# Performance work log

Measured on AMD Instinct MI355X. Metric: run time of the kernel, lower is better.

The kernel has to match this reference:

```python
import jax, jax.numpy as jnp
import numpy as np

N = 20000   # num_nodes
D = 128     # node_dim
H = 128     # hidden_dim (also per-head channels, PyG out_channels is per-head)
EV = 64     # event_dim
NH = 4      # heads
E = 250000  # num edges
NT = 8      # num_event_types
K = 4       # active event types


def setup_inputs() -> dict:
    key = jax.random.key(0)
    ks = jax.random.split(key, 24)
    def w(i, shape, s=0.05):
        return jax.random.normal(ks[i], shape, dtype=jnp.float32) * s
    z = lambda shape: jnp.zeros(shape, jnp.float32)
    o = lambda shape: jnp.ones(shape, jnp.float32)
    return {
        "node_ids": jnp.arange(N, dtype=jnp.int32),
        "event_type_ids": jax.random.randint(ks[0], (K,), 0, NT, dtype=jnp.int32),
        "src": jax.random.randint(ks[1], (E,), 0, N, dtype=jnp.int32),
        "dst": jax.random.randint(ks[2], (E,), 0, N, dtype=jnp.int32),
        "event_features": jax.random.normal(ks[3], (EV,), dtype=jnp.float32),
        "event_intensity": jax.random.uniform(ks[4], (K,), dtype=jnp.float32),
        "node_emb_table": w(5, (N, D), 1.0),
        "event_type_table": w(6, (NT, H), 0.5),
        "ev_w1": w(7, (EV, H)), "ev_b1": z((H,)), "ev_g1": o((H,)), "ev_bt1": z((H,)),
        "ev_w2": w(8, (H, H)), "ev_b2": z((H,)), "ev_g2": o((H,)), "ev_bt2": z((H,)),
        "wq": w(9, (D + H, NH * H)), "bq": z((NH * H,)),
        "wk": w(10, (D + H, NH * H)), "bk": z((NH * H,)),
        "wv": w(11, (D + H, NH * H)), "bv": z((NH * H,)),
        "wskip": w(12, (D + H, H)), "bskip": z((H,)),
        "g0_w": w(13, (H, NH * H)), "g0_as": w(14, (NH, H), 0.1), "g0_ad": w(15, (NH, H), 0.1), "g0_b": z((H,)),
        "g1_w": w(16, (H, NH * H)), "g1_as": w(17, (NH, H), 0.1), "g1_ad": w(18, (NH, H), 0.1), "g1_b": z((H,)),
        "wih": w(19, (H, 4 * H)), "whh": w(20, (H, 4 * H)), "bih": z((4 * H,)), "bhh": z((4 * H,)),
    }


def layer_norm(x, g, b, eps=1e-5):
    mu = jnp.mean(x, axis=-1, keepdims=True)
    var = jnp.mean(jnp.square(x - mu), axis=-1, keepdims=True)
    return (x - mu) * jax.lax.rsqrt(var + eps) * g + b


def segment_softmax(logits, seg, n):
    # logits: [E, NH]; softmax over edges sharing the same destination seg id
    m = jax.ops.segment_max(logits, seg, num_segments=n)
    m = jnp.where(jnp.isfinite(m), m, 0.0)  # guard empty segments
    e = jnp.exp(logits - m[seg])
    s = jax.ops.segment_sum(e, seg, num_segments=n)
    return e / (s[seg] + 1e-16)


def _forward(node_ids, event_type_ids, src, dst,
             event_features, event_intensity, node_emb_table, event_type_table,
             ev_w1, ev_b1, ev_g1, ev_bt1, ev_w2, ev_b2, ev_g2, ev_bt2,
             wq, bq, wk, bk, wv, bv, wskip, bskip,
             g0_w, g0_as, g0_ad, g0_b, g1_w, g1_as, g1_ad, g1_b,
             wih, whh, bih, bhh):
    node_emb = node_emb_table[node_ids]                                      # [N, D]
    # event encoder MLP (dropout off / eval mode)
    e = jax.nn.relu(layer_norm(event_features @ ev_w1 + ev_b1, ev_g1, ev_bt1))
    e = jax.nn.relu(layer_norm(e @ ev_w2 + ev_b2, ev_g2, ev_bt2))            # [H]
    # intensity-weighted mean of active event-type embeddings
    e = e + jnp.mean(event_type_table[event_type_ids] * event_intensity[:, None], axis=0)
    x = jnp.concatenate([node_emb, jnp.broadcast_to(e, (N, H))], axis=1)     # [N, D+H]

    # --- TransformerConv (heads=NH, concat=False -> head mean, root_weight skip) ---
    q = (x @ wq + bq).reshape(N, NH, H)
    k = (x @ wk + bk).reshape(N, NH, H)
    v = (x @ wv + bv).reshape(N, NH, H)
    alpha = jnp.sum(q[dst] * k[src], axis=-1) / jnp.sqrt(jnp.float32(H))     # [E, NH]
    alpha = segment_softmax(alpha, dst, N)
    agg = jax.ops.segment_sum(v[src] * alpha[..., None], dst, num_segments=N)  # [N, NH, H]
    x = agg.mean(axis=1) + x @ wskip + bskip                                 # [N, H]

    sl = jnp.arange(N, dtype=src.dtype)
    src2 = jnp.concatenate([src, sl])
    dst2 = jnp.concatenate([dst, sl])
    for w_, asrc, adst, b_ in ((g0_w, g0_as, g0_ad, g0_b), (g1_w, g1_as, g1_ad, g1_b)):
        xh = (x @ w_).reshape(N, NH, H)
        a_s = jnp.sum(xh * asrc, axis=-1)                                    # [N, NH]
        a_d = jnp.sum(xh * adst, axis=-1)
        ee = jax.nn.leaky_relu(a_s[src2] + a_d[dst2], 0.2)                   # [E+N, NH]
        a = segment_softmax(ee, dst2, N)
        out = jax.ops.segment_sum(xh[src2] * a[..., None], dst2, num_segments=N)
        x = jax.nn.relu(out.mean(axis=1) + b_)                               # [N, H]

    # --- batched LSTMCell, zero initial (h, c); torch gate order i, f, g, o ---
    h0 = jnp.zeros((N, H), x.dtype)
    c0 = jnp.zeros((N, H), x.dtype)
    gates = x @ wih + bih + h0 @ whh + bhh                                   # [N, 4H]
    gi, gf, gg, go = jnp.split(gates, 4, axis=-1)
    c = jax.nn.sigmoid(gf) * c0 + jax.nn.sigmoid(gi) * jnp.tanh(gg)
    h = jax.nn.sigmoid(go) * jnp.tanh(c)
    return h, c


def reference(node_ids, event_type_ids, src, dst,
              event_features, event_intensity, node_emb_table, event_type_table,
              ev_w1, ev_b1, ev_g1, ev_bt1, ev_w2, ev_b2, ev_g2, ev_bt2,
              wq, bq, wk, bk, wv, bv, wskip, bskip,
              g0_w, g0_as, g0_ad, g0_b, g1_w, g1_as, g1_ad, g1_b,
              wih, whh, bih, bhh):
    return _forward(node_ids, event_type_ids, src, dst,
                    event_features, event_intensity, node_emb_table, event_type_table,
                    ev_w1, ev_b1, ev_g1, ev_bt1, ev_w2, ev_b2, ev_g2, ev_bt2,
                    wq, bq, wk, bk, wv, bv, wskip, bskip,
                    g0_w, g0_as, g0_ad, g0_b, g1_w, g1_as, g1_ad, g1_b,
                    wih, whh, bih, bhh)
```

## Files before the change

### kernel.cpp

```cpp
#include <hip/hip_runtime.h>
#include <math.h>

#define D_DIM 128
#define H_DIM 128
#define SQRT_H_INV 0.08838834764831845f
#define BCOL_QKV 0
#define BCOL_G0 1664
#define BCOL_G1 2176
#define BCOL_W  2688
#define BCOL_TOT 3072

typedef unsigned short u16;
typedef unsigned int u32;
typedef unsigned short ushort8v __attribute__((ext_vector_type(8)));
typedef unsigned int u32x4 __attribute__((ext_vector_type(4)));
typedef __bf16 bf16x8 __attribute__((ext_vector_type(8)));
typedef float f32x4 __attribute__((ext_vector_type(4)));
typedef float f32x2 __attribute__((ext_vector_type(2)));


__device__ __forceinline__ float grp16_sum(float v) {
  v += __shfl_xor(v, 1);
  v += __shfl_xor(v, 2);
  v += __shfl_xor(v, 4);
  v += __shfl_xor(v, 8);
  return v;
}

__device__ __forceinline__ void split_bf16(float x, u16& h, u16& l) {
  __bf16 hb = (__bf16)x;
  float rm = x - (float)hb;
  __bf16 lb = (__bf16)rm;
  h = __builtin_bit_cast(u16, hb);
  l = __builtin_bit_cast(u16, lb);
}

__device__ __forceinline__ f32x2 cvt2(u32 v) {
  f32x2 r;
  r[0] = __builtin_bit_cast(float, v << 16);
  r[1] = __builtin_bit_cast(float, v & 0xffff0000u);
  return r;
}

__device__ __forceinline__ float qk_dot(const u32x4 q, const u32x4 k) {
  float p = 0.f;
  asm("v_dot2_f32_bf16 %0, %1, %2, %0" : "+v"(p) : "v"(q[0]), "v"(k[0]));
  asm("v_dot2_f32_bf16 %0, %1, %2, %0" : "+v"(p) : "v"(q[1]), "v"(k[1]));
  asm("v_dot2_f32_bf16 %0, %1, %2, %0" : "+v"(p) : "v"(q[2]), "v"(k[2]));
  asm("v_dot2_f32_bf16 %0, %1, %2, %0" : "+v"(p) : "v"(q[3]), "v"(k[3]));
  return p;
}

__global__ __launch_bounds__(128) void k_event(
    const float* __restrict__ ef, int EV,
    const float* __restrict__ w1, const float* __restrict__ b1,
    const float* __restrict__ g1, const float* __restrict__ bt1,
    const float* __restrict__ w2, const float* __restrict__ b2,
    const float* __restrict__ g2, const float* __restrict__ bt2,
    const float* __restrict__ ett, const int* __restrict__ etid,
    const float* __restrict__ inten, int K,
    float* __restrict__ e_out)
{
  __shared__ float sh[H_DIM];
  __shared__ float red[H_DIM];
  const int t = threadIdx.x;

  float acc = b1[t];
  for (int i = 0; i < EV; ++i) acc += ef[i] * w1[i * H_DIM + t];

  red[t] = acc; __syncthreads();
  for (int s = 64; s > 0; s >>= 1) { if (t < s) red[t] += red[t + s]; __syncthreads(); }
  float mu = red[0] / H_DIM; __syncthreads();
  float d = acc - mu;
  red[t] = d * d; __syncthreads();
  for (int s = 64; s > 0; s >>= 1) { if (t < s) red[t] += red[t + s]; __syncthreads(); }
  float var = red[0] / H_DIM; __syncthreads();
  float y = d * rsqrtf(var + 1e-5f) * g1[t] + bt1[t];
  y = fmaxf(y, 0.f);
  sh[t] = y; __syncthreads();

  float acc2 = b2[t];
  for (int i = 0; i < H_DIM; ++i) acc2 += sh[i] * w2[i * H_DIM + t];

  red[t] = acc2; __syncthreads();
  for (int s = 64; s > 0; s >>= 1) { if (t < s) red[t] += red[t + s]; __syncthreads(); }
  mu = red[0] / H_DIM; __syncthreads();
  d = acc2 - mu;
  red[t] = d * d; __syncthreads();
  for (int s = 64; s > 0; s >>= 1) { if (t < s) red[t] += red[t + s]; __syncthreads(); }
  var = red[0] / H_DIM; __syncthreads();
  float y2 = d * rsqrtf(var + 1e-5f) * g2[t] + bt2[t];
  y2 = fmaxf(y2, 0.f);

  float m = 0.f;
  for (int k = 0; k < K; ++k) m += ett[etid[k] * H_DIM + t] * inten[k];
  e_out[t] = y2 + m / (float)K;
}

__global__ __launch_bounds__(256) void k_cvec_all(
    const float* __restrict__ e,
    const float* __restrict__ wq, const float* __restrict__ bq,
    const float* __restrict__ wk, const float* __restrict__ bk,
    const float* __restrict__ wv, const float* __restrict__ bv,
    const float* __restrict__ wskip, const float* __restrict__ bskip,
    const float* __restrict__ bih, const float* __restrict__ bhh,
    float* __restrict__ cvec1, float* __restrict__ cvec2)
{
  __shared__ float es[H_DIM];
  const int t = threadIdx.x;
  if (t < H_DIM) es[t] = e[t];
  __syncthreads();
  int j = blockIdx.x * 256 + t;
  if (j < 1664) {
    const float* W; const float* b; int col; int stride;
    if (j < 512)       { W = wq;    b = bq;    col = j;        stride = 512; }
    else if (j < 1024) { W = wk;    b = bk;    col = j - 512;  stride = 512; }
    else if (j < 1536) { W = wv;    b = bv;    col = j - 1024; stride = 512; }
    else               { W = wskip; b = bskip; col = j - 1536; stride = 128; }
    float a = b[col];
    for (int i = 0; i < H_DIM; ++i) a += es[i] * W[(D_DIM + i) * stride + col];
    cvec1[j] = a;
  } else if (j < 1664 + 384) {
    int j2 = j - 1664;
    int src = (j2 < 128) ? j2 : j2 + 128;
    cvec2[j2] = bih[src] + bhh[src];
  }
}

__global__ __launch_bounds__(256) void k_split_all(
    const float* __restrict__ wq, const float* __restrict__ wk,
    const float* __restrict__ wv, const float* __restrict__ wskip,
    const float* __restrict__ g0w, const float* __restrict__ g1w,
    const float* __restrict__ wih,
    u16* __restrict__ hi, u16* __restrict__ lo)
{
  int idx = blockIdx.x * 256 + threadIdx.x;
  if (idx >= BCOL_TOT * 16) return;
  int n = idx >> 4, g = idx & 15;
  const float* W; int col, stride;
  if (n < 512)        { W = wq;    col = n;        stride = 512; }
  else if (n < 1024)  { W = wk;    col = n - 512;  stride = 512; }
  else if (n < 1536)  { W = wv;    col = n - 1024; stride = 512; }
  else if (n < 1664)  { W = wskip; col = n - 1536; stride = 128; }
  else if (n < 2176)  { W = g0w;   col = n - 1664; stride = 512; }
  else if (n < 2688)  { W = g1w;   col = n - 2176; stride = 512; }
  else { int c = n - 2688; W = wih; col = (c < 128) ? c : c + 128; stride = 512; }
  size_t dst = (size_t)(n >> 4) * 2048 + g * 128 + (n & 15) * 8;
#pragma unroll
  for (int j = 0; j < 8; ++j) {
    u16 h, l;
    split_bf16(W[(size_t)(g * 8 + j) * stride + col], h, l);
    hi[dst + j] = h; lo[dst + j] = l;
  }
}

__global__ __launch_bounds__(256) void k_split_a(
    const float* __restrict__ A, const int* __restrict__ ids,
    u16* __restrict__ hi, u16* __restrict__ lo, int M, int Mpad)
{
  int idx = blockIdx.x * 256 + threadIdx.x;
  if (idx >= Mpad * 16) return;
  int row = idx >> 4, g = idx & 15;
  size_t dst = (size_t)(row >> 4) * 2048 + g * 128 + (row & 15) * 8;
  if (row < M) {
    int ar = ids ? ids[row] : row;
    const float* srcp = A + (size_t)ar * 128 + g * 8;
#pragma unroll
    for (int j = 0; j < 8; ++j) {
      u16 h, l;
      split_bf16(srcp[j], h, l);
      hi[dst + j] = h; lo[dst + j] = l;
    }
  } else {
#pragma unroll
    for (int j = 0; j < 8; ++j) { hi[dst + j] = 0; lo[dst + j] = 0; }
  }
}

__global__ __launch_bounds__(256, 3) void mfma_gemm(
    const u16* __restrict__ Ahi, const u16* __restrict__ Alo,
    const u16* __restrict__ Bhi, const u16* __restrict__ Blo,
    const float* __restrict__ cvec,
    u16* __restrict__ bf_out, int bf_cols,
    float* __restrict__ f32_out, int f32_lo, int ld_f32,
    const float* __restrict__ asw, const float* __restrict__ adw,
    float* __restrict__ a_s, float* __restrict__ a_d,
    int M)
{
  __shared__ float red[256];

  const int t = threadIdx.x;
  const int bm = blockIdx.y * 128;
  const int bn = blockIdx.x * 128;
  const int lane = t & 63;
  const int wid = t >> 6;
  const int wr = wid >> 1, wc = wid & 1;
  const int lg = lane >> 4;
  const int lr = lane & 15;

  const int arb = (bm >> 4) + wr * 4;
  const int brb = (bn >> 4) + wc * 4;

  f32x4 acc[4][4];
  const f32x4 zero = {0.f, 0.f, 0.f, 0.f};
#pragma unroll
  for (int i = 0; i < 4; ++i)
#pragma unroll
    for (int j = 0; j < 4; ++j) acc[i][j] = zero;

#pragma unroll
  for (int ks = 0; ks < 4; ++ks) {
    const int g = ks * 4 + lg;
    bf16x8 ah[4], al[4], bh[4], bl[4];
#pragma unroll
    for (int i = 0; i < 4; ++i) {
      size_t oa = (size_t)(arb + i) * 2048 + g * 128 + lr * 8;
      ah[i] = *(const bf16x8*)&Ahi[oa];
      al[i] = *(const bf16x8*)&Alo[oa];
      size_t ob = (size_t)(brb + i) * 2048 + g * 128 + lr * 8;
      bh[i] = *(const bf16x8*)&Bhi[ob];
      bl[i] = *(const bf16x8*)&Blo[ob];
    }
#pragma unroll
    for (int i = 0; i < 4; ++i)
#pragma unroll
      for (int j = 0; j < 4; ++j) {
        acc[i][j] = __builtin_amdgcn_mfma_f32_16x16x32_bf16(ah[i], bh[j], acc[i][j], 0, 0, 0);
        acc[i][j] = __builtin_amdgcn_mfma_f32_16x16x32_bf16(ah[i], bl[j], acc[i][j], 0, 0, 0);
        acc[i][j] = __builtin_amdgcn_mfma_f32_16x16x32_bf16(al[i], bh[j], acc[i][j], 0, 0, 0);
      }
  }

  const int rq = (lane >> 4) << 2;
  const int cq = lane & 15;
  const int head = bn >> 7;

  float ws_[4], wd_[4];
  if (asw) {
#pragma unroll
    for (int j = 0; j < 4; ++j) {
      int cc = (wc * 64 + j * 16 + cq) & 127;
      ws_[j] = asw[head * 128 + cc];
      wd_[j] = adw[head * 128 + cc];
    }
    if (t < 256) red[t] = 0.f;
    __syncthreads();
  }

#pragma unroll
  for (int i = 0; i < 4; ++i) {
#pragma unroll
    for (int r = 0; r < 4; ++r) {
      int rowl = wr * 64 + i * 16 + rq + r;
      int row = bm + rowl;
      bool rok = row < M;
      float ps = 0.f, pd = 0.f;
#pragma unroll
      for (int j = 0; j < 4; ++j) {
        int col = bn + wc * 64 + j * 16 + cq;
        float a = acc[i][j][r];
        if (rok) {
          float val = a + (cvec ? cvec[col] : 0.f);
          if (bf_out && col < bf_cols)
            bf_out[(size_t)row * bf_cols + col] =
                __builtin_bit_cast(u16, (__bf16)val);
          if (f32_out && col >= f32_lo)
            f32_out[(size_t)row * ld_f32 + (col - f32_lo)] = val;
        }
        if (asw) { ps += a * ws_[j]; pd += a * wd_[j]; }
      }
      if (asw && rok) {
        atomicAdd(&red[rowl], ps);
        atomicAdd(&red[128 + rowl], pd);
      }
    }
  }
  if (asw) {
    __syncthreads();
    if (t < 128) {
      int row = bm + t;
      if (row < M) {
        a_s[row * 4 + head] = red[t];
        a_d[row * 4 + head] = red[128 + t];
      }
    }
  }
}

__global__ __launch_bounds__(256) void k_zero(int* __restrict__ p, int n) {
  int i = blockIdx.x * 256 + threadIdx.x;
  if (i < n) p[i] = 0;
}
__global__ __launch_bounds__(256) void k_count(
    const int* __restrict__ dst, int* __restrict__ counts, int E) {
  int e = blockIdx.x * 256 + threadIdx.x;
  if (e < E) atomicAdd(&counts[dst[e]], 1);
}
__global__ __launch_bounds__(1024) void k_scan(
    const int* __restrict__ counts, int* __restrict__ offs,
    int* __restrict__ cursor, int N)
{
  __shared__ int wsum[16];
  const int t = threadIdx.x;
  const int lane = t & 63;
  const int wid = t >> 6;
  int running = 0;
  for (int base = 0; base < N; base += 1024) {
    int v = (base + t < N) ? counts[base + t] : 0;
    int incl = v;
#pragma unroll
    for (int s = 1; s < 64; s <<= 1) {
      int u = __shfl_up(incl, s);
      if (lane >= s) incl += u;
    }
    if (lane == 63) wsum[wid] = incl;
    __syncthreads();
    if (wid == 0) {
      int w = (lane < 16) ? wsum[lane] : 0;
#pragma unroll
      for (int s = 1; s < 16; s <<= 1) {
        int u = __shfl_up(w, s);
        if (lane >= s) w += u;
      }
      if (lane < 16) wsum[lane] = w;
    }
    __syncthreads();
    int wpre = (wid > 0) ? wsum[wid - 1] : 0;
    int tot = wsum[15];
    int inclg = incl + wpre;
    if (base + t < N) {
      offs[base + t + 1] = running + inclg;
      cursor[base + t] = running + inclg - v;
    }
    running += tot;
    __syncthreads();
  }
  if (t == 0) offs[0] = 0;
}
__global__ __launch_bounds__(256) void k_fill(
    const int* __restrict__ src, const int* __restrict__ dst,
    int* __restrict__ cursor, int* __restrict__ csr_src, int E) {
  int e = blockIdx.x * 256 + threadIdx.x;
  if (e < E) {
    int slot = atomicAdd(&cursor[dst[e]], 1);
    csr_src[slot] = src[e];
  }
}

__global__ __launch_bounds__(256) void k_tconv(
    const u16* __restrict__ QKVp, const float* __restrict__ skipbuf,
    const int* __restrict__ offs, const int* __restrict__ csr_src,
    u16* __restrict__ Xhi, u16* __restrict__ Xlo, int N)
{
  const int wid = threadIdx.x >> 6;
  const int lane = threadIdx.x & 63;
  const int node = blockIdx.x * 4 + wid;
  if (node >= N) {
    if (lane < 16) {
      size_t dst = (size_t)(node >> 4) * 2048 + lane * 128 + (node & 15) * 8;
#pragma unroll
      for (int j = 0; j < 8; ++j) { Xhi[dst + j] = 0; Xlo[dst + j] = 0; }
    }
    return;
  }
  const u32x4 q = *(const u32x4*)(QKVp + (size_t)node * 1536 + lane * 8);

  const int beg = offs[node], end = offs[node + 1];
  float mx = -1e30f;
  float ssum = 0.f;
  f32x2 acc2[4];
#pragma unroll
  for (int jj = 0; jj < 4; ++jj) acc2[jj] = (f32x2){0.f, 0.f};

  int e = beg;
  for (; e + 4 <= end; e += 4) {
    int s0 = csr_src[e];
    int s1 = csr_src[e + 1];
    int s2 = csr_src[e + 2];
    int s3 = csr_src[e + 3];
    const u16* r0 = QKVp + (size_t)s0 * 1536 + 512 + lane * 8;
    const u16* r1 = QKVp + (size_t)s1 * 1536 + 512 + lane * 8;
    const u16* r2 = QKVp + (size_t)s2 * 1536 + 512 + lane * 8;
    const u16* r3 = QKVp + (size_t)s3 * 1536 + 512 + lane * 8;
    u32x4 k0 = *(const u32x4*)(r0);
    u32x4 k1 = *(const u32x4*)(r1);
    u32x4 k2 = *(const u32x4*)(r2);
    u32x4 k3 = *(const u32x4*)(r3);
    u32x4 v0 = *(const u32x4*)(r0 + 512);
    u32x4 v1 = *(const u32x4*)(r1 + 512);
    u32x4 v2 = *(const u32x4*)(r2 + 512);
    u32x4 v3 = *(const u32x4*)(r3 + 512);
    float p0 = qk_dot(q, k0);
    float p1 = qk_dot(q, k1);
    float p2 = qk_dot(q, k2);
    float p3 = qk_dot(q, k3);
    p0 = grp16_sum(p0) * SQRT_H_INV;
    p1 = grp16_sum(p1) * SQRT_H_INV;
    p2 = grp16_sum(p2) * SQRT_H_INV;
    p3 = grp16_sum(p3) * SQRT_H_INV;
    float pmax = fmaxf(fmaxf(p0, p1), fmaxf(p2, p3));
    if (!__all(pmax <= mx)) {
      float nm = fmaxf(mx, pmax);
      float sc = expf(mx - nm);
      f32x2 sc2 = {sc, sc};
      ssum *= sc;
#pragma unroll
      for (int jj = 0; jj < 4; ++jj) acc2[jj] *= sc2;
      mx = nm;
    }
    float w0 = expf(p0 - mx);
    float w1 = expf(p1 - mx);
    float w2 = expf(p2 - mx);
    float w3 = expf(p3 - mx);
    ssum += (w0 + w1) + (w2 + w3);
    f32x2 w02 = {w0, w0}, w12 = {w1, w1}, w22 = {w2, w2}, w32 = {w3, w3};
#pragma unroll
    for (int jj = 0; jj < 4; ++jj)
      acc2[jj] = acc2[jj] + (w02 * cvt2(v0[jj]) + w12 * cvt2(v1[jj]))
                          + (w22 * cvt2(v2[jj]) + w32 * cvt2(v3[jj]));
  }
  for (; e < end; ++e) {
    int s0 = csr_src[e];
    const u16* r0 = QKVp + (size_t)s0 * 1536 + 512 + lane * 8;
    u32x4 k0 = *(const u32x4*)(r0);
    u32x4 v0 = *(const u32x4*)(r0 + 512);
    float p0 = qk_dot(q, k0);
    p0 = grp16_sum(p0) * SQRT_H_INV;
    if (!__all(p0 <= mx)) {
      float nm = fmaxf(mx, p0);
      float sc = expf(mx - nm);
      f32x2 sc2 = {sc, sc};
      ssum *= sc;
#pragma unroll
      for (int jj = 0; jj < 4; ++jj) acc2[jj] *= sc2;
      mx = nm;
    }
    float w0 = expf(p0 - mx);
    ssum += w0;
    f32x2 w02 = {w0, w0};
#pragma unroll
    for (int jj = 0; jj < 4; ++jj)
      acc2[jj] = acc2[jj] + w02 * cvt2(v0[jj]);
  }

  float inv = 1.f / (ssum + 1e-16f);
  float acc[8];
#pragma unroll
  for (int jj = 0; jj < 4; ++jj) {
    acc[jj * 2]     = acc2[jj][0] * inv;
    acc[jj * 2 + 1] = acc2[jj][1] * inv;
  }
#pragma unroll
  for (int j = 0; j < 8; ++j) {
    acc[j] += __shfl_xor(acc[j], 16);
    acc[j] += __shfl_xor(acc[j], 32);
  }
  if (lane < 16) {
    const float* sk = skipbuf + (size_t)node * 128 + lane * 8;
    size_t dst = (size_t)(node >> 4) * 2048 + lane * 128 + (node & 15) * 8;
#pragma unroll
    for (int j = 0; j < 8; ++j) {
      float x = 0.25f * acc[j] + sk[j];
      u16 h, l;
      split_bf16(x, h, l);
      Xhi[dst + j] = h; Xlo[dst + j] = l;
    }
  }
}

__global__ __launch_bounds__(256) void k_gat_agg(
    const u16* __restrict__ xhb,
    const float* __restrict__ a_s, const float* __restrict__ a_d,
    const int* __restrict__ offs, const int* __restrict__ csr_src,
    const float* __restrict__ bias,
    u16* __restrict__ Xhi, u16* __restrict__ Xlo, int N)
{
  const int wid = threadIdx.x >> 6;
  const int lane = threadIdx.x & 63;
  const int node = blockIdx.x * 4 + wid;
  if (node >= N) {
    if (lane < 16) {
      size_t dst = (size_t)(node >> 4) * 2048 + lane * 128 + (node & 15) * 8;
#pragma unroll
      for (int j = 0; j < 8; ++j) { Xhi[dst + j] = 0; Xlo[dst + j] = 0; }
    }
    return;
  }
  const int head = lane >> 4;
  const float adn = a_d[node * 4 + head];
  const float asn = a_s[node * 4 + head];
  float lself = asn + adn;
  lself = lself >= 0.f ? lself : 0.2f * lself;

  float mx = lself;
  float ssum = 1.f;
  f32x2 acc2[4];
  {
    u32x4 xs = *(const u32x4*)(xhb + (size_t)node * 512 + lane * 8);
#pragma unroll
    for (int jj = 0; jj < 4; ++jj) acc2[jj] = cvt2(xs[jj]);
  }

  const int beg = offs[node], end = offs[node + 1];
  int e = beg;
  for (; e + 4 <= end; e += 4) {
    int s0 = csr_src[e];
    int s1 = csr_src[e + 1];
    int s2 = csr_src[e + 2];
    int s3 = csr_src[e + 3];
    float l0 = a_s[s0 * 4 + head];
    float l1 = a_s[s1 * 4 + head];
    float l2 = a_s[s2 * 4 + head];
    float l3 = a_s[s3 * 4 + head];
    const u16* r0 = xhb + (size_t)s0 * 512 + lane * 8;
    const u16* r1 = xhb + (size_t)s1 * 512 + lane * 8;
    const u16* r2 = xhb + (size_t)s2 * 512 + lane * 8;
    const u16* r3 = xhb + (size_t)s3 * 512 + lane * 8;
    u32x4 xa = *(const u32x4*)(r0);
    u32x4 xb = *(const u32x4*)(r1);
    u32x4 xc = *(const u32x4*)(r2);
    u32x4 xd = *(const u32x4*)(r3);
    l0 += adn; l1 += adn; l2 += adn; l3 += adn;
    l0 = l0 >= 0.f ? l0 : 0.2f * l0;
    l1 = l1 >= 0.f ? l1 : 0.2f * l1;
    l2 = l2 >= 0.f ? l2 : 0.2f * l2;
    l3 = l3 >= 0.f ? l3 : 0.2f * l3;
    float lmax = fmaxf(fmaxf(l0, l1), fmaxf(l2, l3));
    if (!__all(lmax <= mx)) {
      float nm = fmaxf(mx, lmax);
      float sc = expf(mx - nm);
      f32x2 sc2 = {sc, sc};
      ssum *= sc;
#pragma unroll
      for (int jj = 0; jj < 4; ++jj) acc2[jj] *= sc2;
      mx = nm;
    }
    float w0 = expf(l0 - mx);
    float w1 = expf(l1 - mx);
    float w2 = expf(l2 - mx);
    float w3 = expf(l3 - mx);
    ssum += (w0 + w1) + (w2 + w3);
    f32x2 w02 = {w0, w0}, w12 = {w1, w1}, w22 = {w2, w2}, w32 = {w3, w3};
#pragma unroll
    for (int jj = 0; jj < 4; ++jj)
      acc2[jj] = acc2[jj] + (w02 * cvt2(xa[jj]) + w12 * cvt2(xb[jj]))
                          + (w22 * cvt2(xc[jj]) + w32 * cvt2(xd[jj]));
  }
  for (; e < end; ++e) {
    int s0 = csr_src[e];
    float l0 = a_s[s0 * 4 + head] + adn;
    l0 = l0 >= 0.f ? l0 : 0.2f * l0;
    const u16* r0 = xhb + (size_t)s0 * 512 + lane * 8;
    u32x4 xa = *(const u32x4*)(r0);
    if (!__all(l0 <= mx)) {
      float nm = fmaxf(mx, l0);
      float sc = expf(mx - nm);
      f32x2 sc2 = {sc, sc};
      ssum *= sc;
#pragma unroll
      for (int jj = 0; jj < 4; ++jj) acc2[jj] *= sc2;
      mx = nm;
    }
    float w0 = expf(l0 - mx);
    ssum += w0;
    f32x2 w02 = {w0, w0};
#pragma unroll
    for (int jj = 0; jj < 4; ++jj)
      acc2[jj] = acc2[jj] + w02 * cvt2(xa[jj]);
  }

  float inv = 1.f / (ssum + 1e-16f);
  float acc[8];
#pragma unroll
  for (int jj = 0; jj < 4; ++jj) {
    acc[jj * 2]     = acc2[jj][0] * inv;
    acc[jj * 2 + 1] = acc2[jj][1] * inv;
  }
#pragma unroll
  for (int j = 0; j < 8; ++j) {
    acc[j] += __shfl_xor(acc[j], 16);
    acc[j] += __shfl_xor(acc[j], 32);
  }
  if (lane < 16) {
    const float* b = bias + lane * 8;
    size_t dst = (size_t)(node >> 4) * 2048 + lane * 128 + (node & 15) * 8;
#pragma unroll
    for (int j = 0; j < 8; ++j) {
      float x = fmaxf(0.25f * acc[j] + b[j], 0.f);
      u16 h, l;
      split_bf16(x, h, l);
      Xhi[dst + j] = h; Xlo[dst + j] = l;
    }
  }
}

__global__ __launch_bounds__(256) void k_lstm(
    const float* __restrict__ gates, float* __restrict__ out, int N)
{
  int idx = blockIdx.x * 256 + threadIdx.x;
  if (idx >= N * 128) return;
  int n = idx >> 7, c = idx & 127;
  const float* g = gates + (size_t)n * 384;
  float gi = g[c], gg = g[128 + c], go = g[256 + c];
  float cv = (1.f / (1.f + expf(-gi))) * tanhf(gg);
  float hv = (1.f / (1.f + expf(-go))) * tanhf(cv);
  out[idx] = hv;
  out[(size_t)N * 128 + idx] = cv;
}

extern "C" void kernel_launch(void* const* d_in, const int* in_sizes, int n_in,
                              void* d_out, int out_size, void* d_ws, size_t ws_size,
                              hipStream_t stream) {
  const int*   node_ids = (const int*)d_in[0];
  const int*   etid     = (const int*)d_in[1];
  const int*   src      = (const int*)d_in[2];
  const int*   dst      = (const int*)d_in[3];
  const float* ef       = (const float*)d_in[4];
  const float* inten    = (const float*)d_in[5];
  const float* nemb     = (const float*)d_in[6];
  const float* ett      = (const float*)d_in[7];
  const float* ev_w1 = (const float*)d_in[8],  *ev_b1 = (const float*)d_in[9];
  const float* ev_g1 = (const float*)d_in[10], *ev_bt1 = (const float*)d_in[11];
  const float* ev_w2 = (const float*)d_in[12], *ev_b2 = (const float*)d_in[13];
  const float* ev_g2 = (const float*)d_in[14], *ev_bt2 = (const float*)d_in[15];
  const float* wq = (const float*)d_in[16], *bq = (const float*)d_in[17];
  const float* wk = (const float*)d_in[18], *bk = (const float*)d_in[19];
  const float* wv = (const float*)d_in[20], *bv = (const float*)d_in[21];
  const float* wskip = (const float*)d_in[22], *bskip = (const float*)d_in[23];
  const float* g0_w = (const float*)d_in[24], *g0_as = (const float*)d_in[25];
  const float* g0_ad = (const float*)d_in[26], *g0_b = (const float*)d_in[27];
  const float* g1_w = (const float*)d_in[28], *g1_as = (const float*)d_in[29];
  const float* g1_ad = (const float*)d_in[30], *g1_b = (const float*)d_in[31];
  const float* wih = (const float*)d_in[32];
  const float* bih = (const float*)d_in[34], *bhh = (const float*)d_in[35];

  const int N = in_sizes[0];
  const int K = in_sizes[1];
  const int E = in_sizes[2];
  const int EV = in_sizes[4];

  const int gridMy = (N + 127) / 128;
  const int Npad = gridMy * 128;

  float* ws = (float*)d_ws;
  size_t o = 0;
  float* e_vec = ws + o; o += 128;
  float* cvec1 = ws + o; o += 1664;
  float* cvec2 = ws + o; o += 384;
  u16* Ballhi = (u16*)(ws + o); o += (size_t)BCOL_TOT * 64;
  u16* Balllo = (u16*)(ws + o); o += (size_t)BCOL_TOT * 64;
  u16* Ahi  = (u16*)(ws + o); o += (size_t)Npad * 64;
  u16* Alo  = (u16*)(ws + o); o += (size_t)Npad * 64;
  u16* XShi = (u16*)(ws + o); o += (size_t)Npad * 64;
  u16* XSlo = (u16*)(ws + o); o += (size_t)Npad * 64;
  u16* QKVp = (u16*)(ws + o); o += (size_t)Npad * 768;
  float* skipbuf = ws + o; o += (size_t)Npad * 128;
  u16* xhb  = (u16*)(ws + o); o += (size_t)Npad * 256;
  float* gates = ws + o; o += (size_t)Npad * 192;
  float* a_s   = ws + o; o += (size_t)N * 4;
  float* a_d   = ws + o; o += (size_t)N * 4;
  int* counts  = (int*)(ws + o); o += N;
  int* offs    = (int*)(ws + o); o += (size_t)N + 1;
  int* cursor  = (int*)(ws + o); o += N;
  int* csr_src = (int*)(ws + o); o += E;

  float* out = (float*)d_out;
  const int nodeBlocksPad = Npad / 4;

  k_event<<<1, 128, 0, stream>>>(ef, EV, ev_w1, ev_b1, ev_g1, ev_bt1,
                                 ev_w2, ev_b2, ev_g2, ev_bt2,
                                 ett, etid, inten, K, e_vec);
  k_cvec_all<<<8, 256, 0, stream>>>(e_vec, wq, bq, wk, bk, wv, bv,
                                    wskip, bskip, bih, bhh, cvec1, cvec2);
  k_split_all<<<(BCOL_TOT * 16) / 256, 256, 0, stream>>>(
      wq, wk, wv, wskip, g0_w, g1_w, wih, Ballhi, Balllo);
  k_split_a<<<(Npad * 16 + 255) / 256, 256, 0, stream>>>(nemb, node_ids, Ahi, Alo, N, Npad);

  k_zero<<<(N + 255) / 256, 256, 0, stream>>>(counts, N);
  k_count<<<(E + 255) / 256, 256, 0, stream>>>(dst, counts, E);
  k_scan<<<1, 1024, 0, stream>>>(counts, offs, cursor, N);
  k_fill<<<(E + 255) / 256, 256, 0, stream>>>(src, dst, cursor, csr_src, E);

  mfma_gemm<<<dim3(13, gridMy), 256, 0, stream>>>(
      Ahi, Alo, Ballhi + (size_t)BCOL_QKV * 128, Balllo + (size_t)BCOL_QKV * 128,
      cvec1, QKVp, 1536, skipbuf, 1536, 128,
      nullptr, nullptr, nullptr, nullptr, N);

  k_tconv<<<nodeBlocksPad, 256, 0, stream>>>(QKVp, skipbuf, offs, csr_src,
                                             XShi, XSlo, N);

  mfma_gemm<<<dim3(4, gridMy), 256, 0, stream>>>(
      XShi, XSlo, Ballhi + (size_t)BCOL_G0 * 128, Balllo + (size_t)BCOL_G0 * 128,
      nullptr, xhb, 512, nullptr, 0, 0,
      g0_as, g0_ad, a_s, a_d, N);
  k_gat_agg<<<nodeBlocksPad, 256, 0, stream>>>(xhb, a_s, a_d, offs, csr_src,
                                               g0_b, XShi, XSlo, N);

  mfma_gemm<<<dim3(4, gridMy), 256, 0, stream>>>(
      XShi, XSlo, Ballhi + (size_t)BCOL_G1 * 128, Balllo + (size_t)BCOL_G1 * 128,
      nullptr, xhb, 512, nullptr, 0, 0,
      g1_as, g1_ad, a_s, a_d, N);
  k_gat_agg<<<nodeBlocksPad, 256, 0, stream>>>(xhb, a_s, a_d, offs, csr_src,
                                               g1_b, XShi, XSlo, N);

  mfma_gemm<<<dim3(3, gridMy), 256, 0, stream>>>(
      XShi, XSlo, Ballhi + (size_t)BCOL_W * 128, Balllo + (size_t)BCOL_W * 128,
      cvec2, nullptr, 0, gates, 0, 384,
      nullptr, nullptr, nullptr, nullptr, N);
  k_lstm<<<((N * 128) + 255) / 256, 256, 0, stream>>>(gates, out, N);
}
```

Baseline: 461.2 us.

## Use persistent work-stealing waves for attention aggregation kernels

```diff
diff --git a/kernel.cpp b/kernel.cpp
--- a/kernel.cpp
+++ b/kernel.cpp
@@ -49,6 +49,12 @@
   asm("v_dot2_f32_bf16 %0, %1, %2, %0" : "+v"(p) : "v"(q[2]), "v"(k[2]));
   asm("v_dot2_f32_bf16 %0, %1, %2, %0" : "+v"(p) : "v"(q[3]), "v"(k[3]));
   return p;
+}
+
+__device__ __forceinline__ int steal(int* ctr, int lane) {
+  int n = 0;
+  if (lane == 0) n = atomicAdd(ctr, 1);
+  return __shfl(n, 0);
 }
 
 __global__ __launch_bounds__(128) void k_event(
@@ -350,120 +356,113 @@
 __global__ __launch_bounds__(256) void k_tconv(
     const u16* __restrict__ QKVp, const float* __restrict__ skipbuf,
     const int* __restrict__ offs, const int* __restrict__ csr_src,
-    u16* __restrict__ Xhi, u16* __restrict__ Xlo, int N)
-{
-  const int wid = threadIdx.x >> 6;
+    u16* __restrict__ Xhi, u16* __restrict__ Xlo, int N, int Npad,
+    int* __restrict__ wctr)
+{
   const int lane = threadIdx.x & 63;
-  const int node = blockIdx.x * 4 + wid;
-  if (node >= N) {
-    if (lane < 16) {
-      size_t dst = (size_t)(node >> 4) * 2048 + lane * 128 + (node & 15) * 8;
-#pragma unroll
-      for (int j = 0; j < 8; ++j) { Xhi[dst + j] = 0; Xlo[dst + j] = 0; }
-    }
-    return;
-  }
-  const u32x4 q = *(const u32x4*)(QKVp + (size_t)node * 1536 + lane * 8);
-
-  const int beg = offs[node], end = offs[node + 1];
-  float mx = -1e30f;
-  float ssum = 0.f;
-  f32x2 acc2[4];
-#pragma unroll
-  for (int jj = 0; jj < 4; ++jj) acc2[jj] = (f32x2){0.f, 0.f};
-
-  int e = beg;
-  for (; e + 4 <= end; e += 4) {
-    int s0 = csr_src[e];
-    int s1 = csr_src[e + 1];
-    int s2 = csr_src[e + 2];
-    int s3 = csr_src[e + 3];
-    const u16* r0 = QKVp + (size_t)s0 * 1536 + 512 + lane * 8;
-    const u16* r1 = QKVp + (size_t)s1 * 1536 + 512 + lane * 8;
-    const u16* r2 = QKVp + (size_t)s2 * 1536 + 512 + lane * 8;
-    const u16* r3 = QKVp + (size_t)s3 * 1536 + 512 + lane * 8;
-    u32x4 k0 = *(const u32x4*)(r0);
-    u32x4 k1 = *(const u32x4*)(r1);
-    u32x4 k2 = *(const u32x4*)(r2);
-    u32x4 k3 = *(const u32x4*)(r3);
-    u32x4 v0 = *(const u32x4*)(r0 + 512);
-    u32x4 v1 = *(const u32x4*)(r1 + 512);
-    u32x4 v2 = *(const u32x4*)(r2 + 512);
-    u32x4 v3 = *(const u32x4*)(r3 + 512);
-    float p0 = qk_dot(q, k0);
-    float p1 = qk_dot(q, k1);
-    float p2 = qk_dot(q, k2);
-    float p3 = qk_dot(q, k3);
-    p0 = grp16_sum(p0) * SQRT_H_INV;
-    p1 = grp16_sum(p1) * SQRT_H_INV;
-    p2 = grp16_sum(p2) * SQRT_H_INV;
-    p3 = grp16_sum(p3) * SQRT_H_INV;
-    float pmax = fmaxf(fmaxf(p0, p1), fmaxf(p2, p3));
-    if (!__all(pmax <= mx)) {
-      float nm = fmaxf(mx, pmax);
+
+  for (;;) {
+    const int node = steal(wctr, lane);
+    if (node >= Npad) return;
+    if (node >= N) {
+      if (lane < 16) {
+        size_t dst = (size_t)(node >> 4) * 2048 + lane * 128 + (node & 15) * 8;
+#pragma unroll
+        for (int j = 0; j < 8; ++j) { Xhi[dst + j] = 0; Xlo[dst + j] = 0; }
+      }
+      continue;
+    }
+    const u32x4 q = *(const u32x4*)(QKVp + (size_t)node * 1536 + lane * 8);
+
+    const int beg = offs[node], end = offs[node + 1];
+    float mx = -1e30f;
+    float ssum = 0.f;
+    f32x2 acc2[4];
+#pragma unroll
+    for (int jj = 0; jj < 4; ++jj) acc2[jj] = (f32x2){0.f, 0.f};
+
+    int e = beg;
+    for (; e + 4 <= end; e += 4) {
+      int s0 = csr_src[e];
+      int s1 = csr_src[e + 1];
+      int s2 = csr_src[e + 2];
+      int s3 = csr_src[e + 3];
+      const u16* r0 = QKVp + (size_t)s0 * 1536 + 512 + lane * 8;
+      const u16* r1 = QKVp + (size_t)s1 * 1536 + 512 + lane * 8;
+      const u16* r2 = QKVp + (size_t)s2 * 1536 + 512 + lane * 8;
+      const u16* r3 = QKVp + (size_t)s3 * 1536 + 512 + lane * 8;
+      u32x4 k0 = *(const u32x4*)(r0);
+      u32x4 k1 = *(const u32x4*)(r1);
+      u32x4 k2 = *(const u32x4*)(r2);
+      u32x4 k3 = *(const u32x4*)(r3);
+      u32x4 v0 = *(const u32x4*)(r0 + 512);
+      u32x4 v1 = *(const u32x4*)(r1 + 512);
+      u32x4 v2 = *(const u32x4*)(r2 + 512);
+      u32x4 v3 = *(const u32x4*)(r3 + 512);
+      float p0 = qk_dot(q, k0);
+      float p1 = qk_dot(q, k1);
+      float p2 = qk_dot(q, k2);
+      float p3 = qk_dot(q, k3);
+      p0 = grp16_sum(p0) * SQRT_H_INV;
+      p1 = grp16_sum(p1) * SQRT_H_INV;
+      p2 = grp16_sum(p2) * SQRT_H_INV;
+      p3 = grp16_sum(p3) * SQRT_H_INV;
+      float nm = fmaxf(fmaxf(fmaxf(p0, p1), fmaxf(p2, p3)), mx);
       float sc = expf(mx - nm);
+      float w0 = expf(p0 - nm);
+      float w1 = expf(p1 - nm);
+      float w2 = expf(p2 - nm);
+      float w3 = expf(p3 - nm);
+      ssum = ssum * sc + (w0 + w1) + (w2 + w3);
       f32x2 sc2 = {sc, sc};
-      ssum *= sc;
-#pragma unroll
-      for (int jj = 0; jj < 4; ++jj) acc2[jj] *= sc2;
+      f32x2 w02 = {w0, w0}, w12 = {w1, w1}, w22 = {w2, w2}, w32 = {w3, w3};
+#pragma unroll
+      for (int jj = 0; jj < 4; ++jj)
+        acc2[jj] = acc2[jj] * sc2 + (w02 * cvt2(v0[jj]) + w12 * cvt2(v1[jj]))
+                                  + (w22 * cvt2(v2[jj]) + w32 * cvt2(v3[jj]));
       mx = nm;
     }
-    float w0 = expf(p0 - mx);
-    float w1 = expf(p1 - mx);
-    float w2 = expf(p2 - mx);
-    float w3 = expf(p3 - mx);
-    ssum += (w0 + w1) + (w2 + w3);
-    f32x2 w02 = {w0, w0}, w12 = {w1, w1}, w22 = {w2, w2}, w32 = {w3, w3};
-#pragma unroll
-    for (int jj = 0; jj < 4; ++jj)
-      acc2[jj] = acc2[jj] + (w02 * cvt2(v0[jj]) + w12 * cvt2(v1[jj]))
-                          + (w22 * cvt2(v2[jj]) + w32 * cvt2(v3[jj]));
-  }
-  for (; e < end; ++e) {
-    int s0 = csr_src[e];
-    const u16* r0 = QKVp + (size_t)s0 * 1536 + 512 + lane * 8;
-    u32x4 k0 = *(const u32x4*)(r0);
-    u32x4 v0 = *(const u32x4*)(r0 + 512);
-    float p0 = qk_dot(q, k0);
-    p0 = grp16_sum(p0) * SQRT_H_INV;
-    if (!__all(p0 <= mx)) {
+    for (; e < end; ++e) {
+      int s0 = csr_src[e];
+      const u16* r0 = QKVp + (size_t)s0 * 1536 + 512 + lane * 8;
+      u32x4 k0 = *(const u32x4*)(r0);
+      u32x4 v0 = *(const u32x4*)(r0 + 512);
+      float p0 = qk_dot(q, k0);
+      p0 = grp16_sum(p0) * SQRT_H_INV;
       float nm = fmaxf(mx, p0);
       float sc = expf(mx - nm);
+      float w0 = expf(p0 - nm);
+      ssum = ssum * sc + w0;
       f32x2 sc2 = {sc, sc};
-      ssum *= sc;
-#pragma unroll
-      for (int jj = 0; jj < 4; ++jj) acc2[jj] *= sc2;
+      f32x2 w02 = {w0, w0};
+#pragma unroll
+      for (int jj = 0; jj < 4; ++jj)
+        acc2[jj] = acc2[jj] * sc2 + w02 * cvt2(v0[jj]);
       mx = nm;
     }
-    float w0 = expf(p0 - mx);
-    ssum += w0;
-    f32x2 w02 = {w0, w0};
-#pragma unroll
-    for (int jj = 0; jj < 4; ++jj)
-      acc2[jj] = acc2[jj] + w02 * cvt2(v0[jj]);
-  }
-
-  float inv = 1.f / (ssum + 1e-16f);
-  float acc[8];
-#pragma unroll
-  for (int jj = 0; jj < 4; ++jj) {
-    acc[jj * 2]     = acc2[jj][0] * inv;
-    acc[jj * 2 + 1] = acc2[jj][1] * inv;
-  }
-#pragma unroll
-  for (int j = 0; j < 8; ++j) {
-    acc[j] += __shfl_xor(acc[j], 16);
-    acc[j] += __shfl_xor(acc[j], 32);
-  }
-  if (lane < 16) {
-    const float* sk = skipbuf + (size_t)node * 128 + lane * 8;
-    size_t dst = (size_t)(node >> 4) * 2048 + lane * 128 + (node & 15) * 8;
+
+    float inv = 1.f / (ssum + 1e-16f);
+    float acc[8];
+#pragma unroll
+    for (int jj = 0; jj < 4; ++jj) {
+      acc[jj * 2]     = acc2[jj][0] * inv;
+      acc[jj * 2 + 1] = acc2[jj][1] * inv;
+    }
 #pragma unroll
     for (int j = 0; j < 8; ++j) {
-      float x = 0.25f * acc[j] + sk[j];
-      u16 h, l;
-      split_bf16(x, h, l);
-      Xhi[dst + j] = h; Xlo[dst + j] = l;
+      acc[j] += __shfl_xor(acc[j], 16);
+      acc[j] += __shfl_xor(acc[j], 32);
+    }
+    if (lane < 16) {
+      const float* sk = skipbuf + (size_t)node * 128 + lane * 8;
+      size_t dst = (size_t)(node >> 4) * 2048 + lane * 128 + (node & 15) * 8;
+#pragma unroll
+      for (int j = 0; j < 8; ++j) {
+        float x = 0.25f * acc[j] + sk[j];
+        u16 h, l;
+        split_bf16(x, h, l);
+        Xhi[dst + j] = h; Xlo[dst + j] = l;
+      }
     }
   }
 }
@@ -473,123 +472,116 @@
     const float* __restrict__ a_s, const float* __restrict__ a_d,
     const int* __restrict__ offs, const int* __restrict__ csr_src,
     const float* __restrict__ bias,
-    u16* __restrict__ Xhi, u16* __restrict__ Xlo, int N)
-{
-  const int wid = threadIdx.x >> 6;
+    u16* __restrict__ Xhi, u16* __restrict__ Xlo, int N, int Npad,
+    int* __restrict__ wctr)
+{
   const int lane = threadIdx.x & 63;
-  const int node = blockIdx.x * 4 + wid;
-  if (node >= N) {
-    if (lane < 16) {
-      size_t dst = (size_t)(node >> 4) * 2048 + lane * 128 + (node & 15) * 8;
-#pragma unroll
-      for (int j = 0; j < 8; ++j) { Xhi[dst + j] = 0; Xlo[dst + j] = 0; }
-    }
-    return;
-  }
   const int head = lane >> 4;
-  const float adn = a_d[node * 4 + head];
-  const float asn = a_s[node * 4 + head];
-  float lself = asn + adn;
-  lself = lself >= 0.f ? lself : 0.2f * lself;
-
-  float mx = lself;
-  float ssum = 1.f;
-  f32x2 acc2[4];
-  {
-    u32x4 xs = *(const u32x4*)(xhb + (size_t)node * 512 + lane * 8);
-#pragma unroll
-    for (int jj = 0; jj < 4; ++jj) acc2[jj] = cvt2(xs[jj]);
-  }
-
-  const int beg = offs[node], end = offs[node + 1];
-  int e = beg;
-  for (; e + 4 <= end; e += 4) {
-    int s0 = csr_src[e];
-    int s1 = csr_src[e + 1];
-    int s2 = csr_src[e + 2];
-    int s3 = csr_src[e + 3];
-    float l0 = a_s[s0 * 4 + head];
-    float l1 = a_s[s1 * 4 + head];
-    float l2 = a_s[s2 * 4 + head];
-    float l3 = a_s[s3 * 4 + head];
-    const u16* r0 = xhb + (size_t)s0 * 512 + lane * 8;
-    const u16* r1 = xhb + (size_t)s1 * 512 + lane * 8;
-    const u16* r2 = xhb + (size_t)s2 * 512 + lane * 8;
-    const u16* r3 = xhb + (size_t)s3 * 512 + lane * 8;
-    u32x4 xa = *(const u32x4*)(r0);
-    u32x4 xb = *(const u32x4*)(r1);
-    u32x4 xc = *(const u32x4*)(r2);
-    u32x4 xd = *(const u32x4*)(r3);
-    l0 += adn; l1 += adn; l2 += adn; l3 += adn;
-    l0 = l0 >= 0.f ? l0 : 0.2f * l0;
-    l1 = l1 >= 0.f ? l1 : 0.2f * l1;
-    l2 = l2 >= 0.f ? l2 : 0.2f * l2;
-    l3 = l3 >= 0.f ? l3 : 0.2f * l3;
-    float lmax = fmaxf(fmaxf(l0, l1), fmaxf(l2, l3));
-    if (!__all(lmax <= mx)) {
-      float nm = fmaxf(mx, lmax);
+
+  for (;;) {
+    const int node = steal(wctr, lane);
+    if (node >= Npad) return;
+    if (node >= N) {
+      if (lane < 16) {
+        size_t dst = (size_t)(node >> 4) * 2048 + lane * 128 + (node & 15) * 8;
+#pragma unroll
+        for (int j = 0; j < 8; ++j) { Xhi[dst + j] = 0; Xlo[dst + j] = 0; }
+      }
+      continue;
+    }
+    const float adn = a_d[node * 4 + head];
+    const float asn = a_s[node * 4 + head];
+    float lself = asn + adn;
+    lself = lself >= 0.f ? lself : 0.2f * lself;
+
+    float mx = lself;
+    float ssum = 1.f;
+    f32x2 acc2[4];
+    {
+      u32x4 xs = *(const u32x4*)(xhb + (size_t)node * 512 + lane * 8);
+#pragma unroll
+      for (int jj = 0; jj < 4; ++jj) acc2[jj] = cvt2(xs[jj]);
+    }
+
+    const int beg = offs[node], end = offs[node + 1];
+    int e = beg;
+    for (; e + 4 <= end; e += 4) {
+      int s0 = csr_src[e];
+      int s1 = csr_src[e + 1];
+      int s2 = csr_src[e + 2];
+      int s3 = csr_src[e + 3];
+      float l0 = a_s[s0 * 4 + head];
+      float l1 = a_s[s1 * 4 + head];
+      float l2 = a_s[s2 * 4 + head];
+      float l3 = a_s[s3 * 4 + head];
+      const u16* r0 = xhb + (size_t)s0 * 512 + lane * 8;
+      const u16* r1 = xhb + (size_t)s1 * 512 + lane * 8;
+      const u16* r2 = xhb + (size_t)s2 * 512 + lane * 8;
+      const u16* r3 = xhb + (size_t)s3 * 512 + lane * 8;
+      u32x4 xa = *(const u32x4*)(r0);
+      u32x4 xb = *(const u32x4*)(r1);
+      u32x4 xc = *(const u32x4*)(r2);
+      u32x4 xd = *(const u32x4*)(r3);
+      l0 += adn; l1 += adn; l2 += adn; l3 += adn;
+      l0 = l0 >= 0.f ? l0 : 0.2f * l0;
+      l1 = l1 >= 0.f ? l1 : 0.2f * l1;
+      l2 = l2 >= 0.f ? l2 : 0.2f * l2;
+      l3 = l3 >= 0.f ? l3 : 0.2f * l3;
+      float nm = fmaxf(fmaxf(fmaxf(l0, l1), fmaxf(l2, l3)), mx);
       float sc = expf(mx - nm);
+      float w0 = expf(l0 - nm);
+      float w1 = expf(l1 - nm);
+      float w2 = expf(l2 - nm);
+      float w3 = expf(l3 - nm);
+      ssum = ssum * sc + (w0 + w1) + (w2 + w3);
       f32x2 sc2 = {sc, sc};
-      ssum *= sc;
-#pragma unroll
-      for (int jj = 0; jj < 4; ++jj) acc2[jj] *= sc2;
+      f32x2 w02 = {w0, w0}, w12 = {w1, w1}, w22 = {w2, w2}, w32 = {w3, w3};
+#pragma unroll
+      for (int jj = 0; jj < 4; ++jj)
+        acc2[jj] = acc2[jj] * sc2 + (w02 * cvt2(xa[jj]) + w12 * cvt2(xb[jj]))
+                                  + (w22 * cvt2(xc[jj]) + w32 * cvt2(xd[jj]));
       mx = nm;
     }
-    float w0 = expf(l0 - mx);
-    float w1 = expf(l1 - mx);
-    float w2 = expf(l2 - mx);
-    float w3 = expf(l3 - mx);
-    ssum += (w0 + w1) + (w2 + w3);
-    f32x2 w02 = {w0, w0}, w12 = {w1, w1}, w22 = {w2, w2}, w32 = {w3, w3};
-#pragma unroll
-    for (int jj = 0; jj < 4; ++jj)
-      acc2[jj] = acc2[jj] + (w02 * cvt2(xa[jj]) + w12 * cvt2(xb[jj]))
-                          + (w22 * cvt2(xc[jj]) + w32 * cvt2(xd[jj]));
-  }
-  for (; e < end; ++e) {
-    int s0 = csr_src[e];
-    float l0 = a_s[s0 * 4 + head] + adn;
-    l0 = l0 >= 0.f ? l0 : 0.2f * l0;
-    const u16* r0 = xhb + (size_t)s0 * 512 + lane * 8;
-    u32x4 xa = *(const u32x4*)(r0);
-    if (!__all(l0 <= mx)) {
+    for (; e < end; ++e) {
+      int s0 = csr_src[e];
+      float l0 = a_s[s0 * 4 + head] + adn;
+      l0 = l0 >= 0.f ? l0 : 0.2f * l0;
+      const u16* r0 = xhb + (size_t)s0 * 512 + lane * 8;
+      u32x4 xa = *(const u32x4*)(r0);
       float nm = fmaxf(mx, l0);
       float sc = expf(mx - nm);
+      float w0 = expf(l0 - nm);
+      ssum = ssum * sc + w0;
       f32x2 sc2 = {sc, sc};
-      ssum *= sc;
-#pragma unroll
-      for (int jj = 0; jj < 4; ++jj) acc2[jj] *= sc2;
+      f32x2 w02 = {w0, w0};
+#pragma unroll
+      for (int jj = 0; jj < 4; ++jj)
+        acc2[jj] = acc2[jj] * sc2 + w02 * cvt2(xa[jj]);
       mx = nm;
     }
-    float w0 = expf(l0 - mx);
-    ssum += w0;
-    f32x2 w02 = {w0, w0};
-#pragma unroll
-    for (int jj = 0; jj < 4; ++jj)
-      acc2[jj] = acc2[jj] + w02 * cvt2(xa[jj]);
-  }
-
-  float inv = 1.f / (ssum + 1e-16f);
-  float acc[8];
-#pragma unroll
-  for (int jj = 0; jj < 4; ++jj) {
-    acc[jj * 2]     = acc2[jj][0] * inv;
-    acc[jj * 2 + 1] = acc2[jj][1] * inv;
-  }
-#pragma unroll
-  for (int j = 0; j < 8; ++j) {
-    acc[j] += __shfl_xor(acc[j], 16);
-    acc[j] += __shfl_xor(acc[j], 32);
-  }
-  if (lane < 16) {
-    const float* b = bias + lane * 8;
-    size_t dst = (size_t)(node >> 4) * 2048 + lane * 128 + (node & 15) * 8;
+
+    float inv = 1.f / (ssum + 1e-16f);
+    float acc[8];
+#pragma unroll
+    for (int jj = 0; jj < 4; ++jj) {
+      acc[jj * 2]     = acc2[jj][0] * inv;
+      acc[jj * 2 + 1] = acc2[jj][1] * inv;
+    }
 #pragma unroll
     for (int j = 0; j < 8; ++j) {
-      float x = fmaxf(0.25f * acc[j] + b[j], 0.f);
-      u16 h, l;
-      split_bf16(x, h, l);
-      Xhi[dst + j] = h; Xlo[dst + j] = l;
+      acc[j] += __shfl_xor(acc[j], 16);
+      acc[j] += __shfl_xor(acc[j], 32);
+    }
+    if (lane < 16) {
+      const float* b = bias + lane * 8;
+      size_t dst = (size_t)(node >> 4) * 2048 + lane * 128 + (node & 15) * 8;
+#pragma unroll
+      for (int j = 0; j < 8; ++j) {
+        float x = fmaxf(0.25f * acc[j] + b[j], 0.f);
+        u16 h, l;
+        split_bf16(x, h, l);
+        Xhi[dst + j] = h; Xlo[dst + j] = l;
+      }
     }
   }
 }
@@ -660,12 +652,13 @@
   float* a_s   = ws + o; o += (size_t)N * 4;
   float* a_d   = ws + o; o += (size_t)N * 4;
   int* counts  = (int*)(ws + o); o += N;
+  int* wctr    = (int*)(ws + o); o += 4;
   int* offs    = (int*)(ws + o); o += (size_t)N + 1;
   int* cursor  = (int*)(ws + o); o += N;
   int* csr_src = (int*)(ws + o); o += E;
 
   float* out = (float*)d_out;
-  const int nodeBlocksPad = Npad / 4;
+  const int persBlocks = 2048;
 
   k_event<<<1, 128, 0, stream>>>(ef, EV, ev_w1, ev_b1, ev_g1, ev_bt1,
                                  ev_w2, ev_b2, ev_g2, ev_bt2,
@@ -676,7 +669,7 @@
       wq, wk, wv, wskip, g0_w, g1_w, wih, Ballhi, Balllo);
   k_split_a<<<(Npad * 16 + 255) / 256, 256, 0, stream>>>(nemb, node_ids, Ahi, Alo, N, Npad);
 
-  k_zero<<<(N + 255) / 256, 256, 0, stream>>>(counts, N);
+  k_zero<<<(N + 4 + 255) / 256, 256, 0, stream>>>(counts, N + 4);
   k_count<<<(E + 255) / 256, 256, 0, stream>>>(dst, counts, E);
   k_scan<<<1, 1024, 0, stream>>>(counts, offs, cursor, N);
   k_fill<<<(E + 255) / 256, 256, 0, stream>>>(src, dst, cursor, csr_src, E);
@@ -686,22 +679,22 @@
       cvec1, QKVp, 1536, skipbuf, 1536, 128,
       nullptr, nullptr, nullptr, nullptr, N);
 
-  k_tconv<<<nodeBlocksPad, 256, 0, stream>>>(QKVp, skipbuf, offs, csr_src,
-                                             XShi, XSlo, N);
+  k_tconv<<<persBlocks, 256, 0, stream>>>(QKVp, skipbuf, offs, csr_src,
+                                          XShi, XSlo, N, Npad, &wctr[0]);
 
   mfma_gemm<<<dim3(4, gridMy), 256, 0, stream>>>(
       XShi, XSlo, Ballhi + (size_t)BCOL_G0 * 128, Balllo + (size_t)BCOL_G0 * 128,
       nullptr, xhb, 512, nullptr, 0, 0,
       g0_as, g0_ad, a_s, a_d, N);
-  k_gat_agg<<<nodeBlocksPad, 256, 0, stream>>>(xhb, a_s, a_d, offs, csr_src,
-                                               g0_b, XShi, XSlo, N);
+  k_gat_agg<<<persBlocks, 256, 0, stream>>>(xhb, a_s, a_d, offs, csr_src,
+                                            g0_b, XShi, XSlo, N, Npad, &wctr[1]);
 
   mfma_gemm<<<dim3(4, gridMy), 256, 0, stream>>>(
       XShi, XSlo, Ballhi + (size_t)BCOL_G1 * 128, Balllo + (size_t)BCOL_G1 * 128,
       nullptr, xhb, 512, nullptr, 0, 0,
       g1_as, g1_ad, a_s, a_d, N);
-  k_gat_agg<<<nodeBlocksPad, 256, 0, stream>>>(xhb, a_s, a_d, offs, csr_src,
-                                               g1_b, XShi, XSlo, N);
+  k_gat_agg<<<persBlocks, 256, 0, stream>>>(xhb, a_s, a_d, offs, csr_src,
+                                            g1_b, XShi, XSlo, N, Npad, &wctr[2]);
 
   mfma_gemm<<<dim3(3, gridMy), 256, 0, stream>>>(
       XShi, XSlo, Ballhi + (size_t)BCOL_W * 128, Balllo + (size_t)BCOL_W * 128,
```

Result: slower. 1.301 ms (+182.1%).
